# Kernel tuning notes

Measured on AMD Instinct MI355X. Metric: run time of the kernel, lower is better.

## Reference

```python
import jax, jax.numpy as jnp
import numpy as np

N_EDGES = 400000
N_GRAPHS = 64
D_FEAT = 128          # width of src / dst / edge_attr / u
D_IN = 4 * D_FEAT     # node_emb_size = 512 (concat width)
D_HID = 256           # hidden_emb_size
D_OUT = 128           # edge_emb_size
SOFTPLUS_THRESH = 20.0


def _softplus(x):
    # torch.nn.Softplus(beta=1, threshold=20): identity for x > 20
    return jnp.where(x > SOFTPLUS_THRESH, x, jax.nn.softplus(x))


def setup_inputs() -> dict:
    key = jax.random.key(0)
    ks = jax.random.split(key, 11)
    src = jax.random.normal(ks[0], (N_EDGES, D_FEAT), dtype=jnp.float32)
    dst = jax.random.normal(ks[1], (N_EDGES, D_FEAT), dtype=jnp.float32)
    edge_attr = jax.random.normal(ks[2], (N_EDGES, D_FEAT), dtype=jnp.float32)
    u = jax.random.normal(ks[3], (N_GRAPHS, D_FEAT), dtype=jnp.float32)
    batch = jax.random.randint(ks[4], (N_EDGES,), 0, N_GRAPHS, dtype=jnp.int64)
    # MLP params (kaiming-uniform-like scale)
    W1 = jax.random.normal(ks[5], (D_IN, D_HID), dtype=jnp.float32) * (1.0 / np.sqrt(D_IN))
    b1 = jax.random.normal(ks[6], (D_HID,), dtype=jnp.float32) * 0.01
    W2 = jax.random.normal(ks[7], (D_HID, D_HID), dtype=jnp.float32) * (1.0 / np.sqrt(D_HID))
    b2 = jax.random.normal(ks[8], (D_HID,), dtype=jnp.float32) * 0.01
    W3 = jax.random.normal(ks[9], (D_HID, D_OUT), dtype=jnp.float32) * (1.0 / np.sqrt(D_HID))
    b3 = jax.random.normal(ks[10], (D_OUT,), dtype=jnp.float32) * 0.01
    return {"src": src, "dst": dst, "edge_attr": edge_attr, "u": u, "batch": batch,
            "W1": W1, "b1": b1, "W2": W2, "b2": b2, "W3": W3, "b3": b3}


def reference(src, dst, edge_attr, u, batch, W1, b1, W2, b2, W3, b3):
    # gather per-graph global features to edges, concat along feature dim
    x = jnp.concatenate([src, dst, edge_attr, u[batch]], axis=1)  # [E, 512]
    h = _softplus(x @ W1 + b1)   # [E, 256]
    h = _softplus(h @ W2 + b2)   # [E, 256]
    return h @ W3 + b3           # [E, 128]
```

## Files before the change

### kernel.cpp

```cpp
#include <hip/hip_runtime.h>
#include <hip/hip_bf16.h>


#define N_EDGE 400000
#define D_FEAT 128
#define D_HID  256
#define D_OUTW 128
#define M_TILE 64

using bf16   = __bf16;
using bf16x4 = __attribute__((ext_vector_type(4))) bf16;
using bf16x8 = __attribute__((ext_vector_type(8))) bf16;
using f32x4  = __attribute__((ext_vector_type(4))) float;

#define FENCE() asm volatile("" ::: "memory")
#define BARRIER() do { FENCE(); __builtin_amdgcn_s_barrier(); FENCE(); } while (0)
#define LGKM0_BARRIER() do { asm volatile("s_waitcnt lgkmcnt(0)" ::: "memory"); \
                             __builtin_amdgcn_s_barrier(); FENCE(); } while (0)

__device__ __forceinline__ unsigned short f2bf(float x) {
  unsigned u = __float_as_uint(x);
  unsigned r = u + 0x7FFFu + ((u >> 16) & 1u);
  return (unsigned short)(r >> 16);
}

__device__ __forceinline__ float softplus_t(float x) {
  float sp = __logf(1.0f + __expf(x));
  return x > 20.0f ? x : sp;
}

__global__ void prep_weights(const float* __restrict__ W1,
                             const float* __restrict__ W2,
                             const float* __restrict__ W3,
                             short* __restrict__ wt) {
  __shared__ float tile[32][33];
  int b = blockIdx.x;
  const float* W; short* Wt; int K, N, kt, nt;
  if (b < 128)      { W = W1; Wt = wt;          K = 512; N = 256; kt = b & 15;  nt = b >> 4; }
  else if (b < 192) { int bb = b - 128; W = W2; Wt = wt + 131072; K = 256; N = 256; kt = bb & 7; nt = bb >> 3; }
  else              { int bb = b - 192; W = W3; Wt = wt + 196608; K = 256; N = 128; kt = bb & 7; nt = bb >> 3; }
  int tx = threadIdx.x, ty = threadIdx.y;
#pragma unroll
  for (int i = 0; i < 4; ++i) {
    int k = kt * 32 + ty + i * 8;
    tile[ty + i * 8][tx] = W[k * N + nt * 32 + tx];
  }
  __syncthreads();
#pragma unroll
  for (int i = 0; i < 4; ++i) {
    int n = nt * 32 + ty + i * 8;
    Wt[n * K + kt * 32 + tx] = (short)f2bf(tile[tx][ty + i * 8]);
  }
}


__global__ __launch_bounds__(256, 3) void edge_mlp(
    const float* __restrict__ src, const float* __restrict__ dst,
    const float* __restrict__ eattr, const float* __restrict__ u,
    const int* __restrict__ batch,
    const float* __restrict__ b1, const float* __restrict__ b2,
    const float* __restrict__ b3,
    const short* __restrict__ wt1, const short* __restrict__ wt2,
    const short* __restrict__ wt3,
    float* __restrict__ out) {
  __shared__ bf16 xs[M_TILE * 128];
  __shared__ bf16 hs[M_TILE * 256];

  const bf16* w1 = (const bf16*)wt1;
  const bf16* w2 = (const bf16*)wt2;
  const bf16* w3 = (const bf16*)wt3;

  const int tid  = threadIdx.x;
  const int wave = tid >> 6;
  const int lane = tid & 63;
  const int quad = lane >> 4;
  const int l16  = lane & 15;
  const int e0   = blockIdx.x * M_TILE;

  const int sm = tid >> 2;
  const int sq = tid & 3;
  const int sb = batch[e0 + sm];

  f32x4 acc[4][4];
#pragma unroll
  for (int i = 0; i < 4; ++i)
#pragma unroll
    for (int j = 0; j < 4; ++j) acc[i][j] = (f32x4)(0.0f);

  f32x4 pf[8];
  {
    const float* base = src + (size_t)(e0 + sm) * D_FEAT;
#pragma unroll
    for (int f = 0; f < 8; ++f) pf[f] = *(const f32x4*)(base + 4 * (sq + 4 * f));
  }

#pragma unroll
  for (int c = 0; c < 4; ++c) {
    bf16x4 pk[8];
#pragma unroll
    for (int f = 0; f < 8; ++f) {
      pk[f][0] = (bf16)pf[f][0]; pk[f][1] = (bf16)pf[f][1];
      pk[f][2] = (bf16)pf[f][2]; pk[f][3] = (bf16)pf[f][3];
    }
    if (c < 3) {
      const float* base;
      if (c == 0)      base = dst   + (size_t)(e0 + sm) * D_FEAT;
      else if (c == 1) base = eattr + (size_t)(e0 + sm) * D_FEAT;
      else             base = u     + (size_t)sb * D_FEAT;
#pragma unroll
      for (int f = 0; f < 8; ++f) pf[f] = *(const f32x4*)(base + 4 * (sq + 4 * f));
    }
    BARRIER();
#pragma unroll
    for (int f = 0; f < 8; ++f) {
      int col = 4 * (sq + 4 * f);
      int g   = col >> 3;
      int off = sm * 128 + (((g ^ (sm & 7)) << 3) + (col & 7));
      *(bf16x4*)&xs[off] = pk[f];
    }
    LGKM0_BARRIER();

    __builtin_amdgcn_s_setprio(1);
#pragma unroll
    for (int ks = 0; ks < 4; ++ks) {
      int kg = c * 128 + ks * 32 + quad * 8;
      bf16x8 a[4], bfr[4];
#pragma unroll
      for (int i = 0; i < 4; ++i)
        a[i] = *(const bf16x8*)(w1 + (wave * 64 + i * 16 + l16) * 512 + kg);
#pragma unroll
      for (int j = 0; j < 4; ++j) {
        int m = j * 16 + l16;
        int g = ks * 4 + quad;
        bfr[j] = *(const bf16x8*)&xs[m * 128 + ((g ^ (m & 7)) << 3)];
      }
#pragma unroll
      for (int i = 0; i < 4; ++i)
#pragma unroll
        for (int j = 0; j < 4; ++j)
          acc[i][j] = __builtin_amdgcn_mfma_f32_16x16x32_bf16(a[i], bfr[j], acc[i][j], 0, 0, 0);
    }
    __builtin_amdgcn_s_setprio(0);
  }

#pragma unroll
  for (int i = 0; i < 4; ++i) {
    int fbase = wave * 64 + i * 16 + quad * 4;
    f32x4 bias = *(const f32x4*)(b1 + fbase);
#pragma unroll
    for (int j = 0; j < 4; ++j) {
      int m = j * 16 + l16;
      bf16x4 p;
#pragma unroll
      for (int r = 0; r < 4; ++r) p[r] = (bf16)softplus_t(acc[i][j][r] + bias[r]);
      int g   = fbase >> 3;
      int off = m * 256 + (((g ^ (m & 7)) << 3) + (fbase & 7));
      *(bf16x4*)&hs[off] = p;
    }
  }
  LGKM0_BARRIER();

  f32x4 acc2[4][4];
#pragma unroll
  for (int i = 0; i < 4; ++i)
#pragma unroll
    for (int j = 0; j < 4; ++j) acc2[i][j] = (f32x4)(0.0f);

  __builtin_amdgcn_s_setprio(1);
#pragma unroll
  for (int ks = 0; ks < 8; ++ks) {
    int kg = ks * 32 + quad * 8;
    bf16x8 a[4], bfr[4];
#pragma unroll
    for (int i = 0; i < 4; ++i)
      a[i] = *(const bf16x8*)(w2 + (wave * 64 + i * 16 + l16) * 256 + kg);
#pragma unroll
    for (int j = 0; j < 4; ++j) {
      int m = j * 16 + l16;
      int g = ks * 4 + quad;
      bfr[j] = *(const bf16x8*)&hs[m * 256 + ((g ^ (m & 7)) << 3)];
    }
#pragma unroll
    for (int i = 0; i < 4; ++i)
#pragma unroll
      for (int j = 0; j < 4; ++j)
        acc2[i][j] = __builtin_amdgcn_mfma_f32_16x16x32_bf16(a[i], bfr[j], acc2[i][j], 0, 0, 0);
  }
  __builtin_amdgcn_s_setprio(0);
  BARRIER();

#pragma unroll
  for (int i = 0; i < 4; ++i) {
    int fbase = wave * 64 + i * 16 + quad * 4;
    f32x4 bias = *(const f32x4*)(b2 + fbase);
#pragma unroll
    for (int j = 0; j < 4; ++j) {
      int m = j * 16 + l16;
      bf16x4 p;
#pragma unroll
      for (int r = 0; r < 4; ++r) p[r] = (bf16)softplus_t(acc2[i][j][r] + bias[r]);
      int g   = fbase >> 3;
      int off = m * 256 + (((g ^ (m & 7)) << 3) + (fbase & 7));
      *(bf16x4*)&hs[off] = p;
    }
  }
  LGKM0_BARRIER();

  const int f0 = (wave & 1) * 64;
  const int m0 = (wave >> 1) * 32;
  f32x4 acc3[4][2];
#pragma unroll
  for (int i = 0; i < 4; ++i)
#pragma unroll
    for (int j = 0; j < 2; ++j) acc3[i][j] = (f32x4)(0.0f);

  __builtin_amdgcn_s_setprio(1);
#pragma unroll
  for (int ks = 0; ks < 8; ++ks) {
    int kg = ks * 32 + quad * 8;
    bf16x8 a[4], bfr[2];
#pragma unroll
    for (int i = 0; i < 4; ++i)
      a[i] = *(const bf16x8*)(w3 + (f0 + i * 16 + l16) * 256 + kg);
#pragma unroll
    for (int j = 0; j < 2; ++j) {
      int m = m0 + j * 16 + l16;
      int g = ks * 4 + quad;
      bfr[j] = *(const bf16x8*)&hs[m * 256 + ((g ^ (m & 7)) << 3)];
    }
#pragma unroll
    for (int i = 0; i < 4; ++i)
#pragma unroll
      for (int j = 0; j < 2; ++j)
        acc3[i][j] = __builtin_amdgcn_mfma_f32_16x16x32_bf16(a[i], bfr[j], acc3[i][j], 0, 0, 0);
  }
  __builtin_amdgcn_s_setprio(0);

#pragma unroll
  for (int i = 0; i < 4; ++i) {
    int fbase = f0 + i * 16 + quad * 4;
    f32x4 bias = *(const f32x4*)(b3 + fbase);
#pragma unroll
    for (int j = 0; j < 2; ++j) {
      int m = m0 + j * 16 + l16;
      f32x4 v = acc3[i][j] + bias;
      *(f32x4*)(out + (size_t)(e0 + m) * D_OUTW + fbase) = v;
    }
  }
}

extern "C" void kernel_launch(void* const* d_in, const int* in_sizes, int n_in,
                              void* d_out, int out_size, void* d_ws, size_t ws_size,
                              hipStream_t stream) {
  const float* src   = (const float*)d_in[0];
  const float* dst   = (const float*)d_in[1];
  const float* eattr = (const float*)d_in[2];
  const float* u     = (const float*)d_in[3];
  const int*   batch = (const int*)d_in[4];
  const float* W1    = (const float*)d_in[5];
  const float* b1    = (const float*)d_in[6];
  const float* W2    = (const float*)d_in[7];
  const float* b2    = (const float*)d_in[8];
  const float* W3    = (const float*)d_in[9];
  const float* b3    = (const float*)d_in[10];
  float* out = (float*)d_out;
  short* wt  = (short*)d_ws;

  prep_weights<<<224, dim3(32, 8), 0, stream>>>(W1, W2, W3, wt);
  edge_mlp<<<N_EDGE / M_TILE, 256, 0, stream>>>(src, dst, eattr, u, batch,
                                                b1, b2, b3,
                                                wt, wt + 131072, wt + 196608, out);
}
```

Baseline: 894.1 us.

## Double-buffer weight fragments across k-steps and layers, alias LDS buffers, raise occupancy

Result: slower. 1.142 ms (+27.7%).

```diff
diff --git a/kernel.cpp b/kernel.cpp
--- a/kernel.cpp
+++ b/kernel.cpp
@@ -54,7 +54,7 @@
 }
 
 
-__global__ __launch_bounds__(256, 3) void edge_mlp(
+__global__ __launch_bounds__(256, 4) void edge_mlp(
     const float* __restrict__ src, const float* __restrict__ dst,
     const float* __restrict__ eattr, const float* __restrict__ u,
     const int* __restrict__ batch,
@@ -63,8 +63,8 @@
     const short* __restrict__ wt1, const short* __restrict__ wt2,
     const short* __restrict__ wt3,
     float* __restrict__ out) {
-  __shared__ bf16 xs[M_TILE * 128];
   __shared__ bf16 hs[M_TILE * 256];
+  bf16* xs = hs;
 
   const bf16* w1 = (const bf16*)wt1;
   const bf16* w2 = (const bf16*)wt2;
@@ -81,6 +81,14 @@
   const int sq = tid & 3;
   const int sb = batch[e0 + sm];
 
+  const bf16* w1r = w1 + (wave * 64 + l16) * 512;
+  const bf16* w2r = w2 + (wave * 64 + l16) * 256;
+  const int   f0  = (wave & 1) * 64;
+  const int   m0  = (wave >> 1) * 32;
+  const bf16* w3r = w3 + (f0 + l16) * 256;
+
+  bf16x8 aw[2][4];
+
   f32x4 acc[4][4];
 #pragma unroll
   for (int i = 0; i < 4; ++i)
@@ -93,6 +101,9 @@
 #pragma unroll
     for (int f = 0; f < 8; ++f) pf[f] = *(const f32x4*)(base + 4 * (sq + 4 * f));
   }
+#pragma unroll
+  for (int i = 0; i < 4; ++i)
+    aw[0][i] = *(const bf16x8*)(w1r + i * 16 * 512 + quad * 8);
 
 #pragma unroll
   for (int c = 0; c < 4; ++c) {
@@ -123,11 +134,20 @@
     __builtin_amdgcn_s_setprio(1);
 #pragma unroll
     for (int ks = 0; ks < 4; ++ks) {
-      int kg = c * 128 + ks * 32 + quad * 8;
-      bf16x8 a[4], bfr[4];
-#pragma unroll
-      for (int i = 0; i < 4; ++i)
-        a[i] = *(const bf16x8*)(w1 + (wave * 64 + i * 16 + l16) * 512 + kg);
+      const int cb = ks & 1, nb = (ks + 1) & 1;
+      if (!(c == 3 && ks == 3)) {
+        int nc = (ks == 3) ? c + 1 : c;
+        int nk = (ks == 3) ? 0 : ks + 1;
+        int kg = nc * 128 + nk * 32 + quad * 8;
+#pragma unroll
+        for (int i = 0; i < 4; ++i)
+          aw[nb][i] = *(const bf16x8*)(w1r + i * 16 * 512 + kg);
+      } else {
+#pragma unroll
+        for (int i = 0; i < 4; ++i)
+          aw[0][i] = *(const bf16x8*)(w2r + i * 16 * 256 + quad * 8);
+      }
+      bf16x8 bfr[4];
 #pragma unroll
       for (int j = 0; j < 4; ++j) {
         int m = j * 16 + l16;
@@ -138,10 +158,12 @@
       for (int i = 0; i < 4; ++i)
 #pragma unroll
         for (int j = 0; j < 4; ++j)
-          acc[i][j] = __builtin_amdgcn_mfma_f32_16x16x32_bf16(a[i], bfr[j], acc[i][j], 0, 0, 0);
+          acc[i][j] = __builtin_amdgcn_mfma_f32_16x16x32_bf16(aw[cb][i], bfr[j], acc[i][j], 0, 0, 0);
     }
     __builtin_amdgcn_s_setprio(0);
   }
+
+  BARRIER();
 
 #pragma unroll
   for (int i = 0; i < 4; ++i) {
@@ -169,11 +191,18 @@
   __builtin_amdgcn_s_setprio(1);
 #pragma unroll
   for (int ks = 0; ks < 8; ++ks) {
-    int kg = ks * 32 + quad * 8;
-    bf16x8 a[4], bfr[4];
-#pragma unroll
-    for (int i = 0; i < 4; ++i)
-      a[i] = *(const bf16x8*)(w2 + (wave * 64 + i * 16 + l16) * 256 + kg);
+    const int cb = ks & 1, nb = (ks + 1) & 1;
+    if (ks < 7) {
+      int kg = (ks + 1) * 32 + quad * 8;
+#pragma unroll
+      for (int i = 0; i < 4; ++i)
+        aw[nb][i] = *(const bf16x8*)(w2r + i * 16 * 256 + kg);
+    } else {
+#pragma unroll
+      for (int i = 0; i < 4; ++i)
+        aw[0][i] = *(const bf16x8*)(w3r + i * 16 * 256 + quad * 8);
+    }
+    bf16x8 bfr[4];
 #pragma unroll
     for (int j = 0; j < 4; ++j) {
       int m = j * 16 + l16;
@@ -184,7 +213,7 @@
     for (int i = 0; i < 4; ++i)
 #pragma unroll
       for (int j = 0; j < 4; ++j)
-        acc2[i][j] = __builtin_amdgcn_mfma_f32_16x16x32_bf16(a[i], bfr[j], acc2[i][j], 0, 0, 0);
+        acc2[i][j] = __builtin_amdgcn_mfma_f32_16x16x32_bf16(aw[cb][i], bfr[j], acc2[i][j], 0, 0, 0);
   }
   __builtin_amdgcn_s_setprio(0);
   BARRIER();
@@ -206,8 +235,6 @@
   }
   LGKM0_BARRIER();
 
-  const int f0 = (wave & 1) * 64;
-  const int m0 = (wave >> 1) * 32;
   f32x4 acc3[4][2];
 #pragma unroll
   for (int i = 0; i < 4; ++i)
@@ -217,11 +244,14 @@
   __builtin_amdgcn_s_setprio(1);
 #pragma unroll
   for (int ks = 0; ks < 8; ++ks) {
-    int kg = ks * 32 + quad * 8;
-    bf16x8 a[4], bfr[2];
-#pragma unroll
-    for (int i = 0; i < 4; ++i)
-      a[i] = *(const bf16x8*)(w3 + (f0 + i * 16 + l16) * 256 + kg);
+    const int cb = ks & 1, nb = (ks + 1) & 1;
+    if (ks < 7) {
+      int kg = (ks + 1) * 32 + quad * 8;
+#pragma unroll
+      for (int i = 0; i < 4; ++i)
+        aw[nb][i] = *(const bf16x8*)(w3r + i * 16 * 256 + kg);
+    }
+    bf16x8 bfr[2];
 #pragma unroll
     for (int j = 0; j < 2; ++j) {
       int m = m0 + j * 16 + l16;
@@ -232,7 +262,7 @@
     for (int i = 0; i < 4; ++i)
 #pragma unroll
       for (int j = 0; j < 2; ++j)
-        acc3[i][j] = __builtin_amdgcn_mfma_f32_16x16x32_bf16(a[i], bfr[j], acc3[i][j], 0, 0, 0);
+        acc3[i][j] = __builtin_amdgcn_mfma_f32_16x16x32_bf16(aw[cb][i], bfr[j], acc3[i][j], 0, 0, 0);
   }
   __builtin_amdgcn_s_setprio(0);
 
```
